# Kernel tuning notes

Hardware: AMD Instinct MI355X
Metric: run time of the kernel (lower is better)

The kernel has to match this reference:

```python
import jax, jax.numpy as jnp
import numpy as np


def binarize_ste(W):
    # sign binarization with straight-through estimator:
    # forward = sign(W) (zeros mapped to +1, standard BNN convention),
    # backward = identity.
    s = jnp.where(W >= 0, 1.0, -1.0).astype(W.dtype)
    return W + jax.lax.stop_gradient(s - W)


def setup_inputs() -> dict:
    key = jax.random.key(0)
    k1, k2 = jax.random.split(key)
    B, N_IN, N_UNITS = 4096, 4096, 4096
    x = jax.random.normal(k1, (B, N_IN), dtype=jnp.float32)
    W = jax.random.normal(k2, (N_IN, N_UNITS), dtype=jnp.float32) * 0.1  # truncated_normal(stddev=0.1) analog
    b = jnp.zeros((N_UNITS,), dtype=jnp.float32)  # constant_initializer(0.0)
    return {"x": x, "W": W, "b": b}


def reference(x, W, b):
    bin_w = binarize_ste(W)           # [n_in, n_units], values in {-1, +1}
    out = x @ bin_w + b               # dense GEMM + bias
    return jax.nn.relu(out)           # act
```

## Files before the change

kernel.cpp:

```cpp
#include <hip/hip_runtime.h>
#include <hip/hip_bf16.h>

typedef unsigned short u16;
typedef signed char i8;
typedef __attribute__((ext_vector_type(4))) int   int4v;
typedef __attribute__((ext_vector_type(4))) float f32x4;

#define GLOBAL_AS __attribute__((address_space(1)))
#define LDS_AS    __attribute__((address_space(3)))

__device__ __forceinline__ void gload_lds16(const void* g, void* l) {
    __builtin_amdgcn_global_load_lds((const GLOBAL_AS unsigned int*)g,
                                     (LDS_AS unsigned int*)l, 16, 0, 0);
}

__global__ __launch_bounds__(256) void quant_x_kernel(const float* __restrict__ X,
                                                      i8* __restrict__ Xq,
                                                      float* __restrict__ inv_s) {
    const int row = blockIdx.x;
    const int t   = threadIdx.x;
    const float4* src = (const float4*)(X + (size_t)row * 4096 + t * 16);
    float4 v0 = src[0], v1 = src[1], v2 = src[2], v3 = src[3];
    float vals[16] = {v0.x, v0.y, v0.z, v0.w, v1.x, v1.y, v1.z, v1.w,
                      v2.x, v2.y, v2.z, v2.w, v3.x, v3.y, v3.z, v3.w};
    float m = 0.f;
#pragma unroll
    for (int j = 0; j < 16; ++j) m = fmaxf(m, fabsf(vals[j]));
#pragma unroll
    for (int off = 32; off; off >>= 1) m = fmaxf(m, __shfl_xor(m, off));
    __shared__ float sm[4];
    if ((t & 63) == 0) sm[t >> 6] = m;
    __syncthreads();
    m = fmaxf(fmaxf(sm[0], sm[1]), fmaxf(sm[2], sm[3]));
    const float s = (m > 0.f) ? 127.0f / m : 0.f;
    uint4 packed;
    unsigned int* pw = (unsigned int*)&packed;
#pragma unroll
    for (int g = 0; g < 4; ++g) {
        unsigned int wd = 0;
#pragma unroll
        for (int j = 0; j < 4; ++j) {
            int q = (int)rintf(vals[g * 4 + j] * s);
            wd |= ((unsigned int)(q & 255)) << (8 * j);
        }
        pw[g] = wd;
    }
    ((uint4*)(Xq + (size_t)row * 4096))[t] = packed;
    if (t == 0) inv_s[row] = m * (1.0f / 127.0f);
}

__global__ __launch_bounds__(256) void conv_w_kernel(const float* __restrict__ W,
                                                     i8* __restrict__ Wt) {
    __shared__ __attribute__((aligned(16))) i8 tile[64][80];
    const int t  = threadIdx.x;
    const int k0 = (blockIdx.x & 63) * 64;
    const int n0 = (blockIdx.x >> 6) * 64;
#pragma unroll
    for (int i = 0; i < 4; ++i) {
        const int r = i * 16 + (t >> 4);
        const int c = (t & 15) * 4;
        float4 v = *(const float4*)&W[(size_t)(k0 + r) * 4096 + n0 + c];
        tile[c + 0][r] = (v.x >= 0.f) ? 1 : -1;
        tile[c + 1][r] = (v.y >= 0.f) ? 1 : -1;
        tile[c + 2][r] = (v.z >= 0.f) ? 1 : -1;
        tile[c + 3][r] = (v.w >= 0.f) ? 1 : -1;
    }
    __syncthreads();
    const int r = t >> 2;
    const int c = (t & 3) * 16;
    *(int4*)&Wt[(size_t)(n0 + r) * 4096 + k0 + c] = *(const int4*)&tile[r][c];
}


#define BAR()        __builtin_amdgcn_s_barrier()
#define LGKM0()      asm volatile("s_waitcnt lgkmcnt(0)")
#define LGKM8()      asm volatile("s_waitcnt lgkmcnt(8)")
#define WAIT_VM4()   asm volatile("s_waitcnt vmcnt(4)" ::: "memory")

#define STAGE_A(bufbase, h, koff)                                                   \
    do {                                                                            \
        const char* _s = Asrc + (size_t)(h) * 524288 + (koff);                      \
        char* _d = lds + (bufbase) + (h) * 16384 + sldsw;                           \
        gload_lds16(_s, _d);                                                        \
        gload_lds16(_s + 262144, _d + 8192);                                        \
    } while (0)
#define STAGE_B(bufbase, h, koff)                                                   \
    do {                                                                            \
        const char* _s = Bsrc + (size_t)(h) * 524288 + (koff);                      \
        char* _d = lds + (bufbase) + 32768 + (h) * 16384 + sldsw;                   \
        gload_lds16(_s, _d);                                                        \
        gload_lds16(_s + 262144, _d + 8192);                                        \
    } while (0)

#define LOAD_A0(bufbase)                                                            \
    do {                                                                            \
        _Pragma("unroll") for (int mi = 0; mi < 4; ++mi)                            \
        _Pragma("unroll") for (int ks = 0; ks < 2; ++ks)                            \
            af0[mi][ks] = *(const int4v*)(lds + (bufbase) + a_rd0 +                 \
                                          mi * 2048 + (rdx ^ (ks * 64)));           \
    } while (0)
#define LOAD_A1(bufbase)                                                            \
    do {                                                                            \
        _Pragma("unroll") for (int mi = 0; mi < 4; ++mi)                            \
        _Pragma("unroll") for (int ks = 0; ks < 2; ++ks)                            \
            af1[mi][ks] = *(const int4v*)(lds + (bufbase) + a_rd0 + 8192 +          \
                                          mi * 2048 + (rdx ^ (ks * 64)));           \
    } while (0)
#define LOAD_B0(bufbase)                                                            \
    do {                                                                            \
        _Pragma("unroll") for (int ni = 0; ni < 2; ++ni)                            \
        _Pragma("unroll") for (int ks = 0; ks < 2; ++ks)                            \
            bf0[ni][ks] = *(const int4v*)(lds + (bufbase) + b_rd0 +                 \
                                          ni * 2048 + (rdx ^ (ks * 64)));           \
    } while (0)
#define LOAD_B1(bufbase)                                                            \
    do {                                                                            \
        _Pragma("unroll") for (int ni = 0; ni < 2; ++ni)                            \
        _Pragma("unroll") for (int ks = 0; ks < 2; ++ks)                            \
            bf1[ni][ks] = *(const int4v*)(lds + (bufbase) + b_rd0 + 4096 +          \
                                          ni * 2048 + (rdx ^ (ks * 64)));           \
    } while (0)

#define MFMA_Q(AF, BF, mq, nq)                                                      \
    do {                                                                            \
        __builtin_amdgcn_s_setprio(1);                                              \
        _Pragma("unroll") for (int mi = 0; mi < 4; ++mi)                            \
        _Pragma("unroll") for (int ni = 0; ni < 2; ++ni)                            \
        _Pragma("unroll") for (int ks = 0; ks < 2; ++ks)                            \
            acc[(mq) * 4 + mi][(nq) * 2 + ni] = __builtin_amdgcn_mfma_i32_16x16x64_i8( \
                AF[mi][ks], BF[ni][ks], acc[(mq) * 4 + mi][(nq) * 2 + ni], 0, 0, 0); \
        __builtin_amdgcn_s_setprio(0);                                              \
    } while (0)

__global__ __launch_bounds__(512, 2) void gemm_bin_kernel(const i8* __restrict__ A,
                                                          const i8* __restrict__ Bt,
                                                          const float* __restrict__ bias,
                                                          const float* __restrict__ inv_s,
                                                          float* __restrict__ C) {
    __shared__ __attribute__((aligned(1024))) char lds[131072];

    const int bid = blockIdx.x;
    const int swz = (bid & 7) * 32 + (bid >> 3);
    const int bm  = swz >> 4;
    const int bn  = swz & 15;

    const int tid = threadIdx.x;
    const int w   = tid >> 6;
    const int l   = tid & 63;
    const int wm  = w >> 2;
    const int wn  = w & 3;

    const int srow = w * 8 + (l >> 3);
    const int scol = ((l & 7) ^ ((l >> 3) & 7)) * 16;
    const char* Asrc = (const char*)A  + (size_t)(bm * 256 + srow) * 4096 + scol;
    const char* Bsrc = (const char*)Bt + (size_t)(bn * 256 + srow) * 4096 + scol;
    const int sldsw = w * 1024;

    const int rdx = (((l >> 4) ^ (l & 7)) << 4);
    const int a_rd0 = wm * 16384 + (l & 15) * 128;
    const int b_rd0 = 32768 + (wn >> 1) * 16384 + (wn & 1) * 8192 + (l & 15) * 128;

    int4v acc[8][4] = {};
    int4v af0[4][2], af1[4][2];
    int4v bf0[2][2], bf1[2][2];

    STAGE_A(0, 0, 0);      STAGE_A(0, 1, 0);
    STAGE_B(0, 0, 0);      STAGE_B(0, 1, 0);
    STAGE_B(65536, 0, 128); STAGE_B(65536, 1, 128);
    WAIT_VM4();
    BAR();

    for (int I = 0; I < 16; ++I) {
        const int koff1 = (2 * I + 1) * 128;
        const int koff2 = ((2 * I + 2) & 31) * 128;
        const int koff3 = ((2 * I + 3) & 31) * 128;

        LOAD_A0(0); LOAD_B0(0); LOAD_B1(0);
        STAGE_A(65536, 0, koff1);
        STAGE_A(65536, 1, koff1);
        LGKM8();
        BAR(); LGKM0();
        MFMA_Q(af0, bf0, 0, 0);
        MFMA_Q(af0, bf1, 0, 1);
        BAR();

        LOAD_A1(0);
        STAGE_B(0, 0, koff2);
        STAGE_B(0, 1, koff2);
        WAIT_VM4();
        BAR(); LGKM0();
        MFMA_Q(af1, bf0, 1, 0);
        MFMA_Q(af1, bf1, 1, 1);
        BAR();

        LOAD_A0(65536); LOAD_B0(65536); LOAD_B1(65536);
        STAGE_A(0, 0, koff2);
        STAGE_A(0, 1, koff2);
        LGKM8();
        BAR(); LGKM0();
        MFMA_Q(af0, bf0, 0, 0);
        MFMA_Q(af0, bf1, 0, 1);
        BAR();

        LOAD_A1(65536);
        STAGE_B(65536, 0, koff3);
        STAGE_B(65536, 1, koff3);
        WAIT_VM4();
        BAR(); LGKM0();
        MFMA_Q(af1, bf0, 1, 0);
        MFMA_Q(af1, bf1, 1, 1);
        BAR();
    }
    asm volatile("s_waitcnt vmcnt(0) lgkmcnt(0)" ::: "memory");

    const int col0 = bn * 256 + wn * 64 + (l & 15);
    const int row0 = bm * 256 + wm * 128 + ((l >> 4) << 2);
    float bn4[4];
#pragma unroll
    for (int n = 0; n < 4; ++n) bn4[n] = bias[col0 + n * 16];
#pragma unroll
    for (int m = 0; m < 8; ++m) {
#pragma unroll
        for (int r = 0; r < 4; ++r) {
            const int  grow = row0 + m * 16 + r;
            const float ivs = inv_s[grow];
#pragma unroll
            for (int n = 0; n < 4; ++n) {
                const float v = (float)acc[m][n][r] * ivs + bn4[n];
                C[(size_t)grow * 4096 + (col0 + n * 16)] = v > 0.f ? v : 0.f;
            }
        }
    }
}

__global__ __launch_bounds__(256) void fallback_kernel(const float* __restrict__ X,
                                                       const float* __restrict__ W,
                                                       const float* __restrict__ b,
                                                       float* __restrict__ out) {
    __shared__ float xs[16][16];
    __shared__ float ws[16][17];
    const int row = blockIdx.y * 16 + threadIdx.y;
    const int col = blockIdx.x * 16 + threadIdx.x;
    float acc = 0.f;
    for (int k0 = 0; k0 < 4096; k0 += 16) {
        xs[threadIdx.y][threadIdx.x] = X[(size_t)row * 4096 + k0 + threadIdx.x];
        float w = W[(size_t)(k0 + threadIdx.y) * 4096 + col];
        ws[threadIdx.y][threadIdx.x] = (w >= 0.f) ? 1.f : -1.f;
        __syncthreads();
#pragma unroll
        for (int kk = 0; kk < 16; ++kk) acc += xs[threadIdx.y][kk] * ws[kk][threadIdx.x];
        __syncthreads();
    }
    const float v = acc + b[col];
    out[(size_t)row * 4096 + col] = v > 0.f ? v : 0.f;
}

extern "C" void kernel_launch(void* const* d_in, const int* in_sizes, int n_in,
                              void* d_out, int out_size, void* d_ws, size_t ws_size,
                              hipStream_t stream) {
    const float* x = (const float*)d_in[0];
    const float* W = (const float*)d_in[1];
    const float* b = (const float*)d_in[2];
    float* out = (float*)d_out;

    const size_t need = (size_t)32 * 1024 * 1024 + 64 * 1024;
    if (ws_size < need) {
        fallback_kernel<<<dim3(256, 256), dim3(16, 16), 0, stream>>>(x, W, b, out);
        return;
    }

    i8*    Xq  = (i8*)d_ws;
    i8*    Wt  = Xq + (size_t)4096 * 4096;
    float* ivs = (float*)(Xq + (size_t)2 * 4096 * 4096);

    quant_x_kernel<<<dim3(4096), dim3(256), 0, stream>>>(x, Xq, ivs);
    conv_w_kernel<<<dim3(4096), dim3(256), 0, stream>>>(W, Wt);
    gemm_bin_kernel<<<dim3(256), dim3(512), 0, stream>>>(Xq, Wt, b, ivs, out);
}
```

Baseline: 93.49 us.

## Retile int8 GEMM to 128x256 blocks with simpler double-buffered K=64 pipeline

Replaces the 256x256-tile, 512-thread GEMM with a 128x256-tile, 256-thread kernel that loops over K in steps of 64. It uses a simple two-buffer LDS ring with one barrier pair per step and a new swizzle for 64-byte rows. The grid doubles to 512 blocks and LDS use drops to 48 KB, so more blocks can share a CU and occupancy rises. In exchange, each block reuses less data, the loop runs 64 iterations instead of 16, and there is less overlap between LDS reads and MFMAs.

```diff
diff --git a/kernel.cpp b/kernel.cpp
--- a/kernel.cpp
+++ b/kernel.cpp
@@ -73,161 +73,99 @@
 
 
 #define BAR()        __builtin_amdgcn_s_barrier()
-#define LGKM0()      asm volatile("s_waitcnt lgkmcnt(0)")
-#define LGKM8()      asm volatile("s_waitcnt lgkmcnt(8)")
-#define WAIT_VM4()   asm volatile("s_waitcnt vmcnt(4)" ::: "memory")
-
-#define STAGE_A(bufbase, h, koff)                                                   \
+#define LGKM0M()     asm volatile("s_waitcnt lgkmcnt(0)" ::: "memory")
+#define WAIT_VM6()   asm volatile("s_waitcnt vmcnt(6)" ::: "memory")
+
+#define STAGE_TILE(bufb, koff)                                                      \
     do {                                                                            \
-        const char* _s = Asrc + (size_t)(h) * 524288 + (koff);                      \
-        char* _d = lds + (bufbase) + (h) * 16384 + sldsw;                           \
-        gload_lds16(_s, _d);                                                        \
-        gload_lds16(_s + 262144, _d + 8192);                                        \
+        gload_lds16(AsrcT + (koff),                     lds + (bufb) + wA);         \
+        gload_lds16(AsrcT + 65536 + (koff),             lds + (bufb) + wA + 1024);  \
+        gload_lds16(BsrcT + (koff),                     lds + (bufb) + 8192 + wB);          \
+        gload_lds16(BsrcT + 65536 + (koff),             lds + (bufb) + 8192 + wB + 1024);   \
+        gload_lds16(BsrcT + 131072 + (koff),            lds + (bufb) + 8192 + wB + 2048);   \
+        gload_lds16(BsrcT + 196608 + (koff),            lds + (bufb) + 8192 + wB + 3072);   \
     } while (0)
-#define STAGE_B(bufbase, h, koff)                                                   \
-    do {                                                                            \
-        const char* _s = Bsrc + (size_t)(h) * 524288 + (koff);                      \
-        char* _d = lds + (bufbase) + 32768 + (h) * 16384 + sldsw;                   \
-        gload_lds16(_s, _d);                                                        \
-        gload_lds16(_s + 262144, _d + 8192);                                        \
-    } while (0)
-
-#define LOAD_A0(bufbase)                                                            \
-    do {                                                                            \
-        _Pragma("unroll") for (int mi = 0; mi < 4; ++mi)                            \
-        _Pragma("unroll") for (int ks = 0; ks < 2; ++ks)                            \
-            af0[mi][ks] = *(const int4v*)(lds + (bufbase) + a_rd0 +                 \
-                                          mi * 2048 + (rdx ^ (ks * 64)));           \
-    } while (0)
-#define LOAD_A1(bufbase)                                                            \
-    do {                                                                            \
-        _Pragma("unroll") for (int mi = 0; mi < 4; ++mi)                            \
-        _Pragma("unroll") for (int ks = 0; ks < 2; ++ks)                            \
-            af1[mi][ks] = *(const int4v*)(lds + (bufbase) + a_rd0 + 8192 +          \
-                                          mi * 2048 + (rdx ^ (ks * 64)));           \
-    } while (0)
-#define LOAD_B0(bufbase)                                                            \
-    do {                                                                            \
-        _Pragma("unroll") for (int ni = 0; ni < 2; ++ni)                            \
-        _Pragma("unroll") for (int ks = 0; ks < 2; ++ks)                            \
-            bf0[ni][ks] = *(const int4v*)(lds + (bufbase) + b_rd0 +                 \
-                                          ni * 2048 + (rdx ^ (ks * 64)));           \
-    } while (0)
-#define LOAD_B1(bufbase)                                                            \
-    do {                                                                            \
-        _Pragma("unroll") for (int ni = 0; ni < 2; ++ni)                            \
-        _Pragma("unroll") for (int ks = 0; ks < 2; ++ks)                            \
-            bf1[ni][ks] = *(const int4v*)(lds + (bufbase) + b_rd0 + 4096 +          \
-                                          ni * 2048 + (rdx ^ (ks * 64)));           \
-    } while (0)
-
-#define MFMA_Q(AF, BF, mq, nq)                                                      \
-    do {                                                                            \
-        __builtin_amdgcn_s_setprio(1);                                              \
-        _Pragma("unroll") for (int mi = 0; mi < 4; ++mi)                            \
-        _Pragma("unroll") for (int ni = 0; ni < 2; ++ni)                            \
-        _Pragma("unroll") for (int ks = 0; ks < 2; ++ks)                            \
-            acc[(mq) * 4 + mi][(nq) * 2 + ni] = __builtin_amdgcn_mfma_i32_16x16x64_i8( \
-                AF[mi][ks], BF[ni][ks], acc[(mq) * 4 + mi][(nq) * 2 + ni], 0, 0, 0); \
-        __builtin_amdgcn_s_setprio(0);                                              \
-    } while (0)
-
-__global__ __launch_bounds__(512, 2) void gemm_bin_kernel(const i8* __restrict__ A,
+
+__global__ __launch_bounds__(256, 2) void gemm_bin_kernel(const i8* __restrict__ A,
                                                           const i8* __restrict__ Bt,
                                                           const float* __restrict__ bias,
                                                           const float* __restrict__ inv_s,
                                                           float* __restrict__ C) {
-    __shared__ __attribute__((aligned(1024))) char lds[131072];
+    __shared__ __attribute__((aligned(1024))) char lds[49152];
 
     const int bid = blockIdx.x;
-    const int swz = (bid & 7) * 32 + (bid >> 3);
+    const int swz = (bid & 7) * 64 + (bid >> 3);
     const int bm  = swz >> 4;
     const int bn  = swz & 15;
 
     const int tid = threadIdx.x;
     const int w   = tid >> 6;
     const int l   = tid & 63;
-    const int wm  = w >> 2;
-    const int wn  = w & 3;
-
-    const int srow = w * 8 + (l >> 3);
-    const int scol = ((l & 7) ^ ((l >> 3) & 7)) * 16;
-    const char* Asrc = (const char*)A  + (size_t)(bm * 256 + srow) * 4096 + scol;
-    const char* Bsrc = (const char*)Bt + (size_t)(bn * 256 + srow) * 4096 + scol;
-    const int sldsw = w * 1024;
-
-    const int rdx = (((l >> 4) ^ (l & 7)) << 4);
-    const int a_rd0 = wm * 16384 + (l & 15) * 128;
-    const int b_rd0 = 32768 + (wn >> 1) * 16384 + (wn & 1) * 8192 + (l & 15) * 128;
-
-    int4v acc[8][4] = {};
-    int4v af0[4][2], af1[4][2];
-    int4v bf0[2][2], bf1[2][2];
-
-    STAGE_A(0, 0, 0);      STAGE_A(0, 1, 0);
-    STAGE_B(0, 0, 0);      STAGE_B(0, 1, 0);
-    STAGE_B(65536, 0, 128); STAGE_B(65536, 1, 128);
-    WAIT_VM4();
+    const int wm  = w >> 1;
+    const int wn  = w & 1;
+
+    const int lin8 = (l & 7) ^ (l >> 3);
+    const int sr2  = (l >> 3) * 2 + (lin8 >> 2);
+    const int sc   = (lin8 & 3) * 16;
+    const char* AsrcT = (const char*)A  + (size_t)(bm * 128 + 32 * w + sr2) * 4096 + sc;
+    const char* BsrcT = (const char*)Bt + (size_t)(bn * 256 + 64 * w + sr2) * 4096 + sc;
+    const int wA = w * 2048;
+    const int wB = w * 4096;
+
+    const int rsl  = ((l >> 4) + 4 * (l & 1)) ^ ((l >> 1) & 7);
+    const int a_rd = wm * 4096 + ((l & 15) >> 1) * 128 + rsl * 16;
+    const int b_rd = 8192 + wn * 8192 + ((l & 15) >> 1) * 128 + rsl * 16;
+
+    int4v acc[4][8] = {};
+    int4v af[4], bf[8];
+
+    STAGE_TILE(0, 0);
+    STAGE_TILE(24576, 64);
+    WAIT_VM6();
     BAR();
 
-    for (int I = 0; I < 16; ++I) {
-        const int koff1 = (2 * I + 1) * 128;
-        const int koff2 = ((2 * I + 2) & 31) * 128;
-        const int koff3 = ((2 * I + 3) & 31) * 128;
-
-        LOAD_A0(0); LOAD_B0(0); LOAD_B1(0);
-        STAGE_A(65536, 0, koff1);
-        STAGE_A(65536, 1, koff1);
-        LGKM8();
-        BAR(); LGKM0();
-        MFMA_Q(af0, bf0, 0, 0);
-        MFMA_Q(af0, bf1, 0, 1);
+    for (int t = 0; t < 64; ++t) {
+        const int bufb  = (t & 1) * 24576;
+        const int koff2 = ((t + 2) & 63) * 64;
+
+#pragma unroll
+        for (int mi = 0; mi < 4; ++mi)
+            af[mi] = *(const int4v*)(lds + bufb + a_rd + mi * 1024);
+#pragma unroll
+        for (int ni = 0; ni < 8; ++ni)
+            bf[ni] = *(const int4v*)(lds + bufb + b_rd + ni * 1024);
+        LGKM0M();
         BAR();
-
-        LOAD_A1(0);
-        STAGE_B(0, 0, koff2);
-        STAGE_B(0, 1, koff2);
-        WAIT_VM4();
-        BAR(); LGKM0();
-        MFMA_Q(af1, bf0, 1, 0);
-        MFMA_Q(af1, bf1, 1, 1);
+        STAGE_TILE(bufb, koff2);
+        WAIT_VM6();
         BAR();
 
-        LOAD_A0(65536); LOAD_B0(65536); LOAD_B1(65536);
-        STAGE_A(0, 0, koff2);
-        STAGE_A(0, 1, koff2);
-        LGKM8();
-        BAR(); LGKM0();
-        MFMA_Q(af0, bf0, 0, 0);
-        MFMA_Q(af0, bf1, 0, 1);
-        BAR();
-
-        LOAD_A1(65536);
-        STAGE_B(65536, 0, koff3);
-        STAGE_B(65536, 1, koff3);
-        WAIT_VM4();
-        BAR(); LGKM0();
-        MFMA_Q(af1, bf0, 1, 0);
-        MFMA_Q(af1, bf1, 1, 1);
-        BAR();
+        __builtin_amdgcn_s_setprio(1);
+#pragma unroll
+        for (int mi = 0; mi < 4; ++mi)
+#pragma unroll
+            for (int ni = 0; ni < 8; ++ni)
+                acc[mi][ni] = __builtin_amdgcn_mfma_i32_16x16x64_i8(af[mi], bf[ni],
+                                                                    acc[mi][ni], 0, 0, 0);
+        __builtin_amdgcn_s_setprio(0);
     }
     asm volatile("s_waitcnt vmcnt(0) lgkmcnt(0)" ::: "memory");
 
-    const int col0 = bn * 256 + wn * 64 + (l & 15);
-    const int row0 = bm * 256 + wm * 128 + ((l >> 4) << 2);
-    float bn4[4];
-#pragma unroll
-    for (int n = 0; n < 4; ++n) bn4[n] = bias[col0 + n * 16];
-#pragma unroll
-    for (int m = 0; m < 8; ++m) {
+    const int col0 = bn * 256 + wn * 128 + (l & 15);
+    const int row0 = bm * 128 + wm * 64 + ((l >> 4) << 2);
+    float bn8[8];
+#pragma unroll
+    for (int ni = 0; ni < 8; ++ni) bn8[ni] = bias[col0 + ni * 16];
+#pragma unroll
+    for (int mi = 0; mi < 4; ++mi) {
 #pragma unroll
         for (int r = 0; r < 4; ++r) {
-            const int  grow = row0 + m * 16 + r;
-            const float ivs = inv_s[grow];
-#pragma unroll
-            for (int n = 0; n < 4; ++n) {
-                const float v = (float)acc[m][n][r] * ivs + bn4[n];
-                C[(size_t)grow * 4096 + (col0 + n * 16)] = v > 0.f ? v : 0.f;
+            const int   grow = row0 + mi * 16 + r;
+            const float ivs  = inv_s[grow];
+#pragma unroll
+            for (int ni = 0; ni < 8; ++ni) {
+                const float v = (float)acc[mi][ni][r] * ivs + bn8[ni];
+                C[(size_t)grow * 4096 + (col0 + ni * 16)] = v > 0.f ? v : 0.f;
             }
         }
     }
@@ -275,5 +213,5 @@
 
     quant_x_kernel<<<dim3(4096), dim3(256), 0, stream>>>(x, Xq, ivs);
     conv_w_kernel<<<dim3(4096), dim3(256), 0, stream>>>(W, Wt);
-    gemm_bin_kernel<<<dim3(256), dim3(512), 0, stream>>>(Xq, Wt, b, ivs, out);
-}
+    gemm_bin_kernel<<<dim3(512), dim3(256), 0, stream>>>(Xq, Wt, b, ivs, out);
+}
```

Measured after the change: 105.6 us. +12.9%, slower.
